# Performance work log

Hardware: AMD Instinct MI355X
Metric: run time of the kernel (lower is better)

The kernel has to match this reference:

```python
import jax, jax.numpy as jnp
import numpy as np

BN_EPS = 1e-5

def conv1x1(x, w, b):
    # x: [B,C,H,W], w: [O,C], b: [O]
    return jnp.einsum('bchw,oc->bohw', x, w) + b[None, :, None, None]

def bn_inf(x, gamma, beta, mean, var):
    inv = gamma / jnp.sqrt(var + BN_EPS)
    return (x - mean[None, :, None, None]) * inv[None, :, None, None] + beta[None, :, None, None]

def setup_inputs() -> dict:
    key = jax.random.key(0)
    ks = jax.random.split(key, 24)
    B, Fg, Fl, Fi = 8, 256, 256, 64
    H = W = 64
    c8 = Fi // 8
    d = {}
    d['g'] = jax.random.normal(ks[0], (B, Fg, H, W), jnp.float32)
    d['x'] = jax.random.normal(ks[1], (B, Fl, H, W), jnp.float32)
    # W_g: conv1x1 + BN
    d['Wg_w'] = jax.random.normal(ks[2], (Fi, Fg), jnp.float32) * (1.0 / np.sqrt(Fg))
    d['Wg_b'] = jax.random.normal(ks[3], (Fi,), jnp.float32) * 0.02
    d['bng_gamma'] = jax.random.uniform(ks[4], (Fi,), jnp.float32, 0.5, 1.5)
    d['bng_beta'] = jax.random.normal(ks[5], (Fi,), jnp.float32) * 0.1
    d['bng_mean'] = jax.random.normal(ks[6], (Fi,), jnp.float32) * 0.1
    d['bng_var'] = jax.random.uniform(ks[7], (Fi,), jnp.float32, 0.5, 1.5)
    # W_x: conv1x1 + BN
    d['Wx_w'] = jax.random.normal(ks[8], (Fi, Fl), jnp.float32) * (1.0 / np.sqrt(Fl))
    d['Wx_b'] = jax.random.normal(ks[9], (Fi,), jnp.float32) * 0.02
    d['bnx_gamma'] = jax.random.uniform(ks[10], (Fi,), jnp.float32, 0.5, 1.5)
    d['bnx_beta'] = jax.random.normal(ks[11], (Fi,), jnp.float32) * 0.1
    d['bnx_mean'] = jax.random.normal(ks[12], (Fi,), jnp.float32) * 0.1
    d['bnx_var'] = jax.random.uniform(ks[13], (Fi,), jnp.float32, 0.5, 1.5)
    # psi: conv1x1 (Fi->1) + BN(1) + sigmoid
    d['psi_w'] = jax.random.normal(ks[14], (1, Fi), jnp.float32) * (1.0 / np.sqrt(Fi))
    d['psi_b'] = jax.random.normal(ks[15], (1,), jnp.float32) * 0.02
    d['bnp_gamma'] = jax.random.uniform(ks[16], (1,), jnp.float32, 0.5, 1.5)
    d['bnp_beta'] = jax.random.normal(ks[17], (1,), jnp.float32) * 0.1
    d['bnp_mean'] = jax.random.normal(ks[18], (1,), jnp.float32) * 0.1
    d['bnp_var'] = jax.random.uniform(ks[19], (1,), jnp.float32, 0.5, 1.5)
    # PAM convs
    d['pb_w'] = jax.random.normal(ks[20], (c8, Fi), jnp.float32) * (1.0 / np.sqrt(Fi))
    d['pb_b'] = jnp.zeros((c8,), jnp.float32)
    d['pc_w'] = jax.random.normal(ks[21], (c8, Fi), jnp.float32) * (1.0 / np.sqrt(Fi))
    d['pc_b'] = jnp.zeros((c8,), jnp.float32)
    d['pd_w'] = jax.random.normal(ks[22], (Fi, Fi), jnp.float32) * (1.0 / np.sqrt(Fi))
    d['pd_b'] = jnp.zeros((Fi,), jnp.float32)
    # scalar gates (torch inits to 0; use small nonzero to exercise the path)
    d['alpha'] = jax.random.normal(ks[23], (1,), jnp.float32) * 0.05
    d['cam_beta'] = jax.random.normal(jax.random.fold_in(key, 99), (1,), jnp.float32) * 0.05
    return d

def _cam(psi, cam_beta):
    B, C, H, W = psi.shape
    feat = psi.reshape(B, C, H * W)                       # [B,C,HW]
    att = jnp.einsum('bcn,bdn->bcd', feat, feat)          # [B,C,C]
    att_new = jnp.max(att, axis=-1, keepdims=True) - att  # max-subtract trick
    att = jax.nn.softmax(att_new, axis=-1)
    out = jnp.einsum('bcd,bdn->bcn', att, feat).reshape(B, C, H, W)
    return cam_beta[0] * out + psi

def _pam(psi, pb_w, pb_b, pc_w, pc_b, pd_w, pd_b, alpha):
    B, C, H, W = psi.shape
    HW = H * W
    fb = conv1x1(psi, pb_w, pb_b).reshape(B, -1, HW)      # [B,C/8,HW]
    fc = conv1x1(psi, pc_w, pc_b).reshape(B, -1, HW)      # [B,C/8,HW]
    energy = jnp.einsum('bki,bkj->bij', fb, fc)           # [B,HW,HW]
    att = jax.nn.softmax(energy, axis=-1)
    fd = conv1x1(psi, pd_w, pd_b).reshape(B, C, HW)       # [B,C,HW]
    out = jnp.einsum('bcj,bij->bci', fd, att).reshape(B, C, H, W)
    return alpha[0] * out + psi

def reference(g, x, Wg_w, Wg_b, bng_gamma, bng_beta, bng_mean, bng_var,
              Wx_w, Wx_b, bnx_gamma, bnx_beta, bnx_mean, bnx_var,
              psi_w, psi_b, bnp_gamma, bnp_beta, bnp_mean, bnp_var,
              pb_w, pb_b, pc_w, pc_b, pd_w, pd_b, alpha, cam_beta):
    g1 = bn_inf(conv1x1(g, Wg_w, Wg_b), bng_gamma, bng_beta, bng_mean, bng_var)
    x1 = bn_inf(conv1x1(x, Wx_w, Wx_b), bnx_gamma, bnx_beta, bnx_mean, bnx_var)
    psi = jax.nn.relu(g1 + x1)                            # [B,F_int,H,W]
    cam = _cam(psi, cam_beta)
    pam = _pam(psi, pb_w, pb_b, pc_w, pc_b, pd_w, pd_b, alpha)
    gate = bn_inf(conv1x1(cam * pam, psi_w, psi_b), bnp_gamma, bnp_beta, bnp_mean, bnp_var)
    da = jax.nn.sigmoid(gate)                             # [B,1,H,W]
    return x * da
```

## Files before the change

kernel.cpp:

```cpp
#include <hip/hip_runtime.h>
#include <hip/hip_bf16.h>
#include <math.h>

#define BB 8
#define CIN 256
#define FI 64
#define HW 4096
#define C8 8
#define EPS 1e-5f
#define LOG2E 1.4426950408889634f

typedef __attribute__((ext_vector_type(8))) short bf16x8;
typedef __attribute__((ext_vector_type(4))) float f32x4;
typedef __attribute__((ext_vector_type(4))) unsigned u32x4;
typedef unsigned short u16;

static __device__ __forceinline__ u16 f2b(float x) {
    unsigned u = __builtin_bit_cast(unsigned, x);
    return (u16)((u + 0x8000u) >> 16);
}
static __device__ __forceinline__ unsigned pk2(float a, float b) {
    unsigned ua = __builtin_bit_cast(unsigned, a);
    unsigned ub = __builtin_bit_cast(unsigned, b);
    return ((ua + 0x8000u) >> 16) | ((ub + 0x8000u) & 0xffff0000u);
}
static __device__ __forceinline__ unsigned cvtpk(float a, float b) {
    unsigned r;
    asm("v_cvt_pk_bf16_f32 %0, %1, %2" : "=v"(r) : "v"(a), "v"(b));
    return r;
}
static __device__ __forceinline__ float b2f(u16 v) {
    return __builtin_bit_cast(float, ((unsigned)v) << 16);
}

__global__ __launch_bounds__(256) void k_prep(
    const float* __restrict__ Wg, const float* __restrict__ Wgb,
    const float* __restrict__ gg, const float* __restrict__ gbeta,
    const float* __restrict__ gm, const float* __restrict__ gv,
    const float* __restrict__ Wx, const float* __restrict__ Wxb,
    const float* __restrict__ xg, const float* __restrict__ xbeta,
    const float* __restrict__ xm, const float* __restrict__ xv,
    const float* __restrict__ pbw, const float* __restrict__ pbb,
    const float* __restrict__ pcw, const float* __restrict__ pcb,
    const float* __restrict__ pdw, const float* __restrict__ pdb,
    u16* __restrict__ Wp, float* __restrict__ Cp,
    u16* __restrict__ Wcat, float* __restrict__ bcat)
{
    const int gid = blockIdx.x * 256 + threadIdx.x;
    for (int idx = gid; idx < FI * 512; idx += 4096) {
        int o = idx >> 9, k = idx & 511;
        float s, w;
        if (k < 256) { s = gg[o] * rsqrtf(gv[o] + EPS); w = Wg[o * 256 + k]; }
        else         { s = xg[o] * rsqrtf(xv[o] + EPS); w = Wx[o * 256 + k - 256]; }
        Wp[idx] = f2b(w * s);
    }
    for (int idx = gid; idx < 80 * 64; idx += 4096) {
        int row = idx >> 6, col = idx & 63;
        float w;
        if (row < 8)       w = pbw[row * 64 + col] * LOG2E;
        else if (row < 16) w = pcw[(row - 8) * 64 + col];
        else               w = pdw[(row - 16) * 64 + col];
        Wcat[idx] = f2b(w);
    }
    if (blockIdx.x == 0) {
        int tid = threadIdx.x;
        if (tid < FI) {
            float ig = gg[tid] * rsqrtf(gv[tid] + EPS);
            float ix = xg[tid] * rsqrtf(xv[tid] + EPS);
            Cp[tid] = (Wgb[tid] - gm[tid]) * ig + gbeta[tid]
                    + (Wxb[tid] - xm[tid]) * ix + xbeta[tid];
        }
        if (tid >= 64 && tid < 144) {
            int r = tid - 64;
            float bv = (r < 8) ? pbb[r] * LOG2E : (r < 16 ? pcb[r - 8] : pdb[r - 16]);
            bcat[r] = bv;
        }
    }
}

__global__ __launch_bounds__(256) void k_psi(
    const float* __restrict__ g, const float* __restrict__ x,
    const u16* __restrict__ Wp, const float* __restrict__ Cp,
    const u16* __restrict__ Wcat, const float* __restrict__ bcat,
    u16* __restrict__ psiB, u16* __restrict__ psiLo,
    u16* __restrict__ fbcT, u16* __restrict__ fdB,
    u16* __restrict__ psiT, u16* __restrict__ psiTLo)
{
    const int tid  = threadIdx.x;
    const int lane = tid & 63;
    const int w    = tid >> 6;
    const int n    = lane & 15;
    const int quad = lane >> 4;
    const int b    = blockIdx.y;
    const int p0   = blockIdx.x * 64;

    __shared__ u16 InT[64][72];
    __shared__ u16 TpH[64][72];
    __shared__ u16 TpL[64][72];
    __shared__ u16 Tbc[64][16];

    f32x4 acc[4];
#pragma unroll
    for (int mt = 0; mt < 4; ++mt) acc[mt] = (f32x4){0.f, 0.f, 0.f, 0.f};

    const size_t pxoff = (size_t)p0 + w * 16 + n;
#pragma unroll
    for (int kc = 0; kc < 8; ++kc) {
        const float* src = (kc < 4) ? g : x;
        const int ch0 = (kc & 3) * 64;
        const float* base = src + ((size_t)b * CIN + ch0 + quad * 8) * HW + pxoff;
#pragma unroll
        for (int ks = 0; ks < 2; ++ks) {
            const float* bp = base + (size_t)(ks * 32) * HW;
            float f0 = bp[0 * HW], f1 = bp[1 * HW], f2 = bp[2 * HW], f3 = bp[3 * HW];
            float f4 = bp[4 * HW], f5 = bp[5 * HW], f6 = bp[6 * HW], f7 = bp[7 * HW];
            u32x4 t = {pk2(f0, f1), pk2(f2, f3), pk2(f4, f5), pk2(f6, f7)};
            bf16x8 bfrag = __builtin_bit_cast(bf16x8, t);
            const int kglob = kc * 64 + ks * 32;
#pragma unroll
            for (int mt = 0; mt < 4; ++mt) {
                bf16x8 af = *(const bf16x8*)&Wp[(mt * 16 + n) * 512 + kglob + quad * 8];
                acc[mt] = __builtin_amdgcn_mfma_f32_16x16x32_bf16(
                              af, bfrag, acc[mt], 0, 0, 0);
            }
        }
    }

    float pv[4][4];
    unsigned hbv[4][4], lov[4][4];
#pragma unroll
    for (int mt = 0; mt < 4; ++mt)
#pragma unroll
        for (int r = 0; r < 4; ++r) {
            int c = mt * 16 + quad * 4 + r;
            float v = acc[mt][r] + Cp[c];
            v = v > 0.f ? v : 0.f;
            pv[mt][r] = v;
            u16 hb = f2b(v);
            u16 lo = f2b(v - b2f(hb));
            hbv[mt][r] = hb;
            lov[mt][r] = lo;
            size_t idx = ((size_t)b * FI + c) * HW + p0 + w * 16 + n;
            psiB[idx]  = hb;
            psiLo[idx] = lo;
        }
#pragma unroll
    for (int mt = 0; mt < 4; ++mt) {
        *(unsigned*)&InT[w * 16 + n][mt * 16 + quad * 4]     = cvtpk(pv[mt][0], pv[mt][1]);
        *(unsigned*)&InT[w * 16 + n][mt * 16 + quad * 4 + 2] = cvtpk(pv[mt][2], pv[mt][3]);
        *(unsigned*)&TpH[w * 16 + n][mt * 16 + quad * 4]     = hbv[mt][0] | (hbv[mt][1] << 16);
        *(unsigned*)&TpH[w * 16 + n][mt * 16 + quad * 4 + 2] = hbv[mt][2] | (hbv[mt][3] << 16);
        *(unsigned*)&TpL[w * 16 + n][mt * 16 + quad * 4]     = lov[mt][0] | (lov[mt][1] << 16);
        *(unsigned*)&TpL[w * 16 + n][mt * 16 + quad * 4 + 2] = lov[mt][2] | (lov[mt][3] << 16);
    }
    __syncthreads();

    if (psiT != nullptr) {
#pragma unroll
        for (int rep = 0; rep < 2; ++rep) {
            int t = rep * 256 + tid;
            int row = t >> 3, seg = t & 7;
            size_t o = ((size_t)b * HW + p0 + row) * 64 + seg * 8;
            *(bf16x8*)&psiT[o]   = *(const bf16x8*)&TpH[row][seg * 8];
            *(bf16x8*)&psiTLo[o] = *(const bf16x8*)&TpL[row][seg * 8];
        }
    }

    f32x4 facc[5];
#pragma unroll
    for (int nt = 0; nt < 5; ++nt) facc[nt] = (f32x4){0.f, 0.f, 0.f, 0.f};
#pragma unroll
    for (int ks = 0; ks < 2; ++ks) {
        bf16x8 af = *(const bf16x8*)&InT[w * 16 + n][ks * 32 + quad * 8];
#pragma unroll
        for (int nt = 0; nt < 5; ++nt) {
            bf16x8 bf = *(const bf16x8*)&Wcat[(nt * 16 + n) * FI + ks * 32 + quad * 8];
            facc[nt] = __builtin_amdgcn_mfma_f32_16x16x32_bf16(af, bf, facc[nt], 0, 0, 0);
        }
    }
    __syncthreads();

    {
        float bias = bcat[n];
#pragma unroll
        for (int r = 0; r < 4; ++r)
            Tbc[w * 16 + quad * 4 + r][n] = f2b(facc[0][r] + bias);
    }
#pragma unroll
    for (int nt = 1; nt < 5; ++nt) {
        int ch = (nt - 1) * 16 + n;
        float bias = bcat[nt * 16 + n];
        *(unsigned*)&InT[ch][w * 16 + quad * 4]     = cvtpk(facc[nt][0] + bias, facc[nt][1] + bias);
        *(unsigned*)&InT[ch][w * 16 + quad * 4 + 2] = cvtpk(facc[nt][2] + bias, facc[nt][3] + bias);
    }
    __syncthreads();
    {
        int row = tid >> 2, part = tid & 3;
        uint2 v = *(const uint2*)&Tbc[row][part * 4];
        *(uint2*)&fbcT[((size_t)b * HW + p0 + row) * 16 + part * 4] = v;
    }
#pragma unroll
    for (int rep = 0; rep < 2; ++rep) {
        int t = rep * 256 + tid;
        int ch = t >> 3, seg = t & 7;
        bf16x8 v = *(const bf16x8*)&InT[ch][seg * 8];
        *(bf16x8*)&fdB[((size_t)b * FI + ch) * HW + p0 + seg * 8] = v;
    }
}

static __device__ __forceinline__ void gram_body(
    int tid, int s, int b, int zz,
    const u16* __restrict__ psiB, const u16* __restrict__ psiLo,
    float* __restrict__ Gp)
{
    const int lane = tid & 63;
    const int w    = tid >> 6;
    const int n    = lane & 15;
    const int quad = lane >> 4;

    f32x4 acc[2];
#pragma unroll
    for (int nt = 0; nt < 2; ++nt) acc[nt] = (f32x4){0.f, 0.f, 0.f, 0.f};

    for (int ks = 0; ks < 4; ++ks) {
        const int k0 = s * 128 + ks * 32;
        const size_t ra = ((size_t)b * FI + w * 16 + n) * HW + k0 + quad * 8;
        bf16x8 ah = *(const bf16x8*)&psiB[ra];
        bf16x8 al = *(const bf16x8*)&psiLo[ra];
#pragma unroll
        for (int nt = 0; nt < 2; ++nt) {
            const size_t rb = ((size_t)b * FI + zz * 32 + nt * 16 + n) * HW + k0 + quad * 8;
            bf16x8 bh = *(const bf16x8*)&psiB[rb];
            bf16x8 bl = *(const bf16x8*)&psiLo[rb];
            acc[nt] = __builtin_amdgcn_mfma_f32_16x16x32_bf16(ah, bh, acc[nt], 0, 0, 0);
            acc[nt] = __builtin_amdgcn_mfma_f32_16x16x32_bf16(ah, bl, acc[nt], 0, 0, 0);
            acc[nt] = __builtin_amdgcn_mfma_f32_16x16x32_bf16(al, bh, acc[nt], 0, 0, 0);
        }
    }
#pragma unroll
    for (int nt = 0; nt < 2; ++nt)
#pragma unroll
        for (int r = 0; r < 4; ++r) {
            int i = w * 16 + quad * 4 + r;
            Gp[(((size_t)s * 8 + b) * 64 + i) * 64 + zz * 32 + nt * 16 + n] = acc[nt][r];
        }
}

struct PamShared {
    u16 Ks[2][68][8];
    u16 Vs[2][64][64];
    u16 Ps[4][16][64];
};

template<int P>
static __device__ __forceinline__ void pam_body(
    PamShared& sh, int tid, int b, int i0, int p,
    const u16* __restrict__ fbcT, const u16* __restrict__ fdB,
    u16* __restrict__ Opart, float* __restrict__ ml)
{
    const int lane = tid & 63;
    const int w    = tid >> 6;
    const int n    = lane & 15;
    const int quad = lane >> 4;
    constexpr int JPER = 64 / P;
    const int jstart = p * JPER, jend = jstart + JPER;

    if (tid < 16) {
        ((unsigned*)&sh.Ks[0][64][0])[tid] = 0u;
        ((unsigned*)&sh.Ks[1][64][0])[tid] = 0u;
    }

    bf16x8 qfrag = {};
    if (quad == 0)
        qfrag = *(const bf16x8*)&fbcT[((size_t)b * HW + i0 + w * 16 + n) * 16];

    const int kkey = tid >> 1, khalf = tid & 1;
    const int vch  = tid >> 3, vseg  = tid & 7;
    const int vslot = (vseg ^ (vch & 7)) << 3;
    const int pswz  = n & 7;

    const u16* kp = fbcT + ((size_t)b * HW + jstart * 64) * 16 + 8;
    const u16* vp = fdB + (size_t)b * FI * HW + jstart * 64;

    uint2 kr0 = make_uint2(0u, 0u), kr1 = make_uint2(0u, 0u);
    bf16x8 v0a, v0b, v1a, v1b;
    if (tid < 128) {
        kr0 = *(const uint2*)(kp + (size_t)kkey * 16 + khalf * 4);
        kr1 = *(const uint2*)(kp + 1024 + (size_t)kkey * 16 + khalf * 4);
    }
    v0a = *(const bf16x8*)(vp + (size_t)vch * HW + vseg * 8);
    v0b = *(const bf16x8*)(vp + (size_t)(32 + vch) * HW + vseg * 8);
    v1a = *(const bf16x8*)(vp + 64 + (size_t)vch * HW + vseg * 8);
    v1b = *(const bf16x8*)(vp + 64 + (size_t)(32 + vch) * HW + vseg * 8);

    f32x4 oacc[4];
#pragma unroll
    for (int mt = 0; mt < 4; ++mt) oacc[mt] = (f32x4){0.f, 0.f, 0.f, 0.f};
    float m = -1e30f, l = 0.f;

#define PAM_STEP(BUF)                                                           \
    {                                                                           \
        f32x4 s[4];                                                             \
        __builtin_amdgcn_s_setprio(1);                                          \
        _Pragma("unroll")                                                       \
        for (int mt = 0; mt < 4; ++mt) {                                        \
            bf16x8 af = *(const bf16x8*)&sh.Ks[BUF][mt * 16 + n + quad][0];     \
            s[mt] = __builtin_amdgcn_mfma_f32_16x16x32_bf16(                    \
                        af, qfrag, (f32x4){0.f, 0.f, 0.f, 0.f}, 0, 0, 0);       \
        }                                                                       \
        __builtin_amdgcn_s_setprio(0);                                          \
        float cm = fmaxf(fmaxf(s[0][0], s[0][1]), s[0][2]);                     \
        cm = fmaxf(fmaxf(cm, s[0][3]), s[1][0]);                                \
        cm = fmaxf(fmaxf(cm, s[1][1]), s[1][2]);                                \
        cm = fmaxf(fmaxf(cm, s[1][3]), s[2][0]);                                \
        cm = fmaxf(fmaxf(cm, s[2][1]), s[2][2]);                                \
        cm = fmaxf(fmaxf(cm, s[2][3]), s[3][0]);                                \
        cm = fmaxf(fmaxf(cm, s[3][1]), s[3][2]);                                \
        cm = fmaxf(cm, s[3][3]);                                                \
        cm = fmaxf(cm, __shfl_xor(cm, 16));                                     \
        cm = fmaxf(cm, __shfl_xor(cm, 32));                                     \
        if (__any(cm > m + 8.f)) {                                              \
            float mnew  = fmaxf(m, cm);                                         \
            float scale = __builtin_amdgcn_exp2f(m - mnew);                     \
            l *= scale;                                                         \
            _Pragma("unroll")                                                   \
            for (int mt = 0; mt < 4; ++mt) {                                    \
                oacc[mt][0] *= scale; oacc[mt][1] *= scale;                     \
                oacc[mt][2] *= scale; oacc[mt][3] *= scale;                     \
            }                                                                   \
            m = mnew;                                                           \
        }                                                                       \
        float psum = 0.f;                                                       \
        unsigned pw[4][2];                                                      \
        _Pragma("unroll")                                                       \
        for (int mt = 0; mt < 4; ++mt) {                                        \
            float e0 = __builtin_amdgcn_exp2f(s[mt][0] - m);                    \
            float e1 = __builtin_amdgcn_exp2f(s[mt][1] - m);                    \
            float e2 = __builtin_amdgcn_exp2f(s[mt][2] - m);                    \
            float e3 = __builtin_amdgcn_exp2f(s[mt][3] - m);                    \
            psum += (e0 + e1) + (e2 + e3);                                      \
            pw[mt][0] = cvtpk(e0, e1);                                          \
            pw[mt][1] = cvtpk(e2, e3);                                          \
        }                                                                       \
        l += psum;                                                              \
        _Pragma("unroll")                                                       \
        for (int mt = 0; mt < 4; ++mt) {                                        \
            int so = (((mt * 2 + (quad >> 1)) ^ pswz) << 3) + ((quad & 1) << 2);\
            *(uint2*)&sh.Ps[w][n][so] = make_uint2(pw[mt][0], pw[mt][1]);       \
        }                                                                       \
        __builtin_amdgcn_s_setprio(1);                                          \
        _Pragma("unroll")                                                       \
        for (int k0 = 0; k0 < 2; ++k0) {                                        \
            bf16x8 pf = *(const bf16x8*)&sh.Ps[w][n][((k0 * 4 + quad) ^ pswz) << 3];\
            _Pragma("unroll")                                                   \
            for (int mt = 0; mt < 4; ++mt) {                                    \
                bf16x8 vf = *(const bf16x8*)                                    \
                    &sh.Vs[BUF][mt * 16 + n][((k0 * 4 + quad) ^ pswz) << 3];    \
                oacc[mt] = __builtin_amdgcn_mfma_f32_16x16x32_bf16(             \
                               vf, pf, oacc[mt], 0, 0, 0);                      \
            }                                                                   \
        }                                                                       \
        __builtin_amdgcn_s_setprio(0);                                          \
    }

    for (int jc = jstart; jc < jend; jc += 2) {
        if (tid < 128) *(uint2*)&sh.Ks[0][kkey][khalf * 4] = kr0;
        *(bf16x8*)&sh.Vs[0][vch][vslot]      = v0a;
        *(bf16x8*)&sh.Vs[0][32 + vch][vslot] = v0b;
        if (jc + 2 < jend) {
            if (tid < 128)
                kr0 = *(const uint2*)(kp + 2048 + (size_t)kkey * 16 + khalf * 4);
            v0a = *(const bf16x8*)(vp + 128 + (size_t)vch * HW + vseg * 8);
            v0b = *(const bf16x8*)(vp + 128 + (size_t)(32 + vch) * HW + vseg * 8);
        }
        __syncthreads();
        PAM_STEP(0)

        if (tid < 128) *(uint2*)&sh.Ks[1][kkey][khalf * 4] = kr1;
        *(bf16x8*)&sh.Vs[1][vch][vslot]      = v1a;
        *(bf16x8*)&sh.Vs[1][32 + vch][vslot] = v1b;
        if (jc + 3 < jend) {
            if (tid < 128)
                kr1 = *(const uint2*)(kp + 3072 + (size_t)kkey * 16 + khalf * 4);
            v1a = *(const bf16x8*)(vp + 192 + (size_t)vch * HW + vseg * 8);
            v1b = *(const bf16x8*)(vp + 192 + (size_t)(32 + vch) * HW + vseg * 8);
        }
        kp += 2048;
        vp += 128;
        __syncthreads();
        PAM_STEP(1)
    }
#undef PAM_STEP

    l += __shfl_xor(l, 16);
    l += __shfl_xor(l, 32);
    const float rl = 1.f / l;
#pragma unroll
    for (int mt = 0; mt < 4; ++mt)
#pragma unroll
        for (int r = 0; r < 4; ++r) {
            int c = mt * 16 + quad * 4 + r;
            Opart[(((size_t)p * 8 + b) * FI + c) * HW + i0 + w * 16 + n] =
                f2b(oacc[mt][r] * rl);
        }
    if (quad == 0)
        ((float2*)ml)[((size_t)p * 8 + b) * HW + i0 + w * 16 + n] = make_float2(m, l);
}

__global__ __launch_bounds__(256) void k_pamgram(
    const u16* __restrict__ fbcT, const u16* __restrict__ fdB,
    const u16* __restrict__ psiB, const u16* __restrict__ psiLo,
    u16* __restrict__ Opart, float* __restrict__ ml, float* __restrict__ Gp)
{
    __shared__ PamShared sh;
    const int bid = blockIdx.x;
    const int tid = threadIdx.x;
    if (bid < 512) {
        gram_body(tid, bid & 31, (bid >> 5) & 7, bid >> 8, psiB, psiLo, Gp);
    } else {
        const int pid = bid - 512;
        pam_body<2>(sh, tid, pid & 7, ((pid >> 3) & 63) * 64, pid >> 9,
                    fbcT, fdB, Opart, ml);
    }
}

__global__ __launch_bounds__(256) void k_gram(
    const u16* __restrict__ psiB, const u16* __restrict__ psiLo,
    float* __restrict__ Gp)
{
    gram_body(threadIdx.x, blockIdx.x, blockIdx.y, blockIdx.z, psiB, psiLo, Gp);
}
__global__ __launch_bounds__(256) void k_pam(
    const u16* __restrict__ fbcT, const u16* __restrict__ fdB,
    u16* __restrict__ Opart, float* __restrict__ ml)
{
    __shared__ PamShared sh;
    pam_body<2>(sh, threadIdx.x, blockIdx.x, blockIdx.y * 64, blockIdx.z,
                fbcT, fdB, Opart, ml);
}

__global__ __launch_bounds__(256) void k_camsm(
    const float* __restrict__ Gp, float* __restrict__ att)
{
    const int tid = threadIdx.x, tx = tid & 63, ty = tid >> 6;
    const int b = blockIdx.x, i = blockIdx.y;
    __shared__ float part[4][64];

    float gs = 0.f;
#pragma unroll
    for (int j = 0; j < 8; ++j) {
        int s = ty * 8 + j;
        gs += Gp[(((size_t)s * 8 + b) * 64 + i) * 64 + tx];
    }
    part[ty][tx] = gs;
    __syncthreads();
    if (tid < 64) {
        float gsum = part[0][tx] + part[1][tx] + part[2][tx] + part[3][tx];
        float M = gsum;
#pragma unroll
        for (int msk = 1; msk < 64; msk <<= 1) M = fmaxf(M, __shfl_xor(M, msk));
        float a = M - gsum;
        float m2 = a;
#pragma unroll
        for (int msk = 1; msk < 64; msk <<= 1) m2 = fmaxf(m2, __shfl_xor(m2, msk));
        float p = __expf(a - m2);
        float ssum = p;
#pragma unroll
        for (int msk = 1; msk < 64; msk <<= 1) ssum += __shfl_xor(ssum, msk);
        att[((size_t)b * 64 + i) * 64 + tx] = p / ssum;
    }
}

__global__ __launch_bounds__(256) void k_final_v(
    const u16* __restrict__ psiT, const u16* __restrict__ psiTLo,
    const float* __restrict__ att,
    const u16* __restrict__ Opart, const float* __restrict__ ml,
    const float* __restrict__ x,
    const float* __restrict__ psiw, const float* __restrict__ psib,
    const float* __restrict__ pg, const float* __restrict__ pbeta,
    const float* __restrict__ pm, const float* __restrict__ pv,
    const float* __restrict__ alpha, const float* __restrict__ camb,
    float* __restrict__ out)
{
    const int tid  = threadIdx.x;
    const int lane = tid & 63;
    const int w    = tid >> 6;
    const int n    = lane & 15;
    const int quad = lane >> 4;
    const int b = blockIdx.y, p0 = blockIdx.x * 32;

    __shared__ u16 Abf[64][64];
    __shared__ u16 tpB[32][64];
    __shared__ u16 tpLo[32][64];
    __shared__ u16 OpS[2][64][40];
    __shared__ float Wc[2][32];
    __shared__ float Pw[64];
    __shared__ alignas(16) float daL[32];
    __shared__ float Zp[4][32];

    {
        int c = tid >> 2, seg = tid & 3;
        const float* ap = &att[((size_t)b * 64 + c) * 64 + seg * 16];
        float4 v0 = *(const float4*)(ap);
        float4 v1 = *(const float4*)(ap + 4);
        float4 v2 = *(const float4*)(ap + 8);
        float4 v3 = *(const float4*)(ap + 12);
        float vv[16] = {v0.x, v0.y, v0.z, v0.w, v1.x, v1.y, v1.z, v1.w,
                        v2.x, v2.y, v2.z, v2.w, v3.x, v3.y, v3.z, v3.w};
#pragma unroll
        for (int j = 0; j < 8; ++j) {
            int d0 = seg * 16 + j * 2;
            int phys = (((d0 >> 3) ^ (c & 7)) << 3) | (d0 & 7);
            *(unsigned*)&Abf[c][phys] = cvtpk(vv[2 * j], vv[2 * j + 1]);
        }
    }
    {
        int row = tid >> 3, seg = tid & 7;
        size_t o = ((size_t)b * HW + p0 + row) * 64 + seg * 8;
        int phys = ((seg ^ (row & 7)) << 3);
        *(bf16x8*)&tpB[row][phys]  = *(const bf16x8*)&psiT[o];
        *(bf16x8*)&tpLo[row][phys] = *(const bf16x8*)&psiTLo[o];
    }
#pragma unroll
    for (int rep = 0; rep < 2; ++rep) {
        int cid = rep * 256 + tid;
        int pp = cid >> 8, c = (cid >> 2) & 63, sg = cid & 3;
        *(bf16x8*)&OpS[pp][c][sg * 8] =
            *(const bf16x8*)&Opart[(((size_t)pp * 8 + b) * FI + c) * HW + p0 + sg * 8];
    }
    if (tid < 64) Pw[tid] = psiw[tid];
    if (tid < 32) {
        float2 ml0 = ((const float2*)ml)[((size_t)0 * 8 + b) * HW + p0 + tid];
        float2 ml1 = ((const float2*)ml)[((size_t)1 * 8 + b) * HW + p0 + tid];
        float M  = fmaxf(ml0.x, ml1.x);
        float w0 = ml0.y * __builtin_amdgcn_exp2f(ml0.x - M);
        float w1 = ml1.y * __builtin_amdgcn_exp2f(ml1.x - M);
        float winv = 1.f / (w0 + w1);
        Wc[0][tid] = w0 * winv; Wc[1][tid] = w1 * winv;
    }
    __syncthreads();

    f32x4 acc[2];
#pragma unroll
    for (int nt = 0; nt < 2; ++nt) acc[nt] = (f32x4){0.f, 0.f, 0.f, 0.f};
#pragma unroll
    for (int ks = 0; ks < 2; ++ks) {
        int arow = w * 16 + n;
        bf16x8 af = *(const bf16x8*)&Abf[arow][((ks * 4 + quad) ^ (arow & 7)) << 3];
#pragma unroll
        for (int nt = 0; nt < 2; ++nt) {
            int brow = nt * 16 + n;
            int boff = ((ks * 4 + quad) ^ (brow & 7)) << 3;
            bf16x8 bh = *(const bf16x8*)&tpB[brow][boff];
            bf16x8 bl = *(const bf16x8*)&tpLo[brow][boff];
            acc[nt] = __builtin_amdgcn_mfma_f32_16x16x32_bf16(af, bh, acc[nt], 0, 0, 0);
            acc[nt] = __builtin_amdgcn_mfma_f32_16x16x32_bf16(af, bl, acc[nt], 0, 0, 0);
        }
    }

    const float al = alpha[0], cb = camb[0];
    float z[2] = {0.f, 0.f};
#pragma unroll
    for (int nt = 0; nt < 2; ++nt) {
        int px = nt * 16 + n;
        float w0 = Wc[0][px], w1 = Wc[1][px];
#pragma unroll
        for (int r = 0; r < 4; ++r) {
            int c = w * 16 + quad * 4 + r;
            int phys = (((c >> 3) ^ (px & 7)) << 3) | (c & 7);
            float ps  = b2f(tpB[px][phys]) + b2f(tpLo[px][phys]);
            float cam = cb * acc[nt][r] + ps;
            float oa = w0 * b2f(OpS[0][c][px]) + w1 * b2f(OpS[1][c][px]);
            float pam = al * oa + ps;
            z[nt] += Pw[c] * (cam * pam);
        }
    }
#pragma unroll
    for (int nt = 0; nt < 2; ++nt) {
        z[nt] += __shfl_xor(z[nt], 16);
        z[nt] += __shfl_xor(z[nt], 32);
    }
    if (quad == 0) {
#pragma unroll
        for (int nt = 0; nt < 2; ++nt) Zp[w][nt * 16 + n] = z[nt];
    }
    __syncthreads();
    if (tid < 32) {
        float zt = Zp[0][tid] + Zp[1][tid] + Zp[2][tid] + Zp[3][tid] + psib[0];
        float inv = pg[0] * rsqrtf(pv[0] + EPS);
        float gate = (zt - pm[0]) * inv + pbeta[0];
        daL[tid] = 1.f / (1.f + __expf(-gate));
    }
    __syncthreads();

    {
        const int pxg = tid & 7, chb = tid >> 3;
        float4 daf = *(const float4*)&daL[pxg * 4];
#pragma unroll
        for (int r = 0; r < 8; ++r) {
            int cl = chb + 32 * r;
            size_t idx = ((size_t)b * CIN + cl) * HW + p0 + pxg * 4;
            float4 xv = *(const float4*)&x[idx];
            *(float4*)&out[idx] = make_float4(xv.x * daf.x, xv.y * daf.y,
                                              xv.z * daf.z, xv.w * daf.w);
        }
    }
}

__global__ __launch_bounds__(256) void k_final_s(
    const u16* __restrict__ psiB, const u16* __restrict__ psiLo,
    const float* __restrict__ att,
    const u16* __restrict__ Opart, const float* __restrict__ ml,
    const float* __restrict__ x,
    const float* __restrict__ psiw, const float* __restrict__ psib,
    const float* __restrict__ pg, const float* __restrict__ pbeta,
    const float* __restrict__ pm, const float* __restrict__ pv,
    const float* __restrict__ alpha, const float* __restrict__ camb,
    float* __restrict__ out)
{
    const int tid  = threadIdx.x;
    const int lane = tid & 63;
    const int w    = tid >> 6;
    const int n    = lane & 15;
    const int quad = lane >> 4;
    const int b = blockIdx.y, p0 = blockIdx.x * 64;

    __shared__ u16 Abf[64][64];
    __shared__ u16 tpB[64][64];
    __shared__ u16 tpLo[64][64];
    __shared__ float Wc0[64], Wc1[64], Pw[64];
    __shared__ alignas(16) float daL[64];
    __shared__ float Zp[4][64];

    {
        int c = tid >> 2, seg = tid & 3;
        const float* ap = &att[((size_t)b * 64 + c) * 64 + seg * 16];
        float4 v0 = *(const float4*)(ap);
        float4 v1 = *(const float4*)(ap + 4);
        float4 v2 = *(const float4*)(ap + 8);
        float4 v3 = *(const float4*)(ap + 12);
        float vv[16] = {v0.x, v0.y, v0.z, v0.w, v1.x, v1.y, v1.z, v1.w,
                        v2.x, v2.y, v2.z, v2.w, v3.x, v3.y, v3.z, v3.w};
#pragma unroll
        for (int j = 0; j < 8; ++j) {
            int d0 = seg * 16 + j * 2;
            int phys = (((d0 >> 3) ^ (c & 7)) << 3) | (d0 & 7);
            *(unsigned*)&Abf[c][phys] = cvtpk(vv[2 * j], vv[2 * j + 1]);
        }
    }
    {
        int px = tid & 63, grp = tid >> 6;
#pragma unroll
        for (int cc = 0; cc < 16; cc += 2) {
            int c = grp * 16 + cc;
            size_t i0 = ((size_t)b * FI + c) * HW + p0 + px;
            unsigned hb = ((unsigned)psiB[i0]) | (((unsigned)psiB[i0 + HW]) << 16);
            unsigned lb = ((unsigned)psiLo[i0]) | (((unsigned)psiLo[i0 + HW]) << 16);
            int phys = (((c >> 3) ^ (px & 7)) << 3) | (c & 7);
            *(unsigned*)&tpB[px][phys]  = hb;
            *(unsigned*)&tpLo[px][phys] = lb;
        }
    }
    if (tid < 64) {
        Pw[tid] = psiw[tid];
        float2 ml0 = ((const float2*)ml)[((size_t)0 * 8 + b) * HW + p0 + tid];
        float2 ml1 = ((const float2*)ml)[((size_t)1 * 8 + b) * HW + p0 + tid];
        float M  = fmaxf(ml0.x, ml1.x);
        float w0 = ml0.y * __builtin_amdgcn_exp2f(ml0.x - M);
        float w1 = ml1.y * __builtin_amdgcn_exp2f(ml1.x - M);
        float winv = 1.f / (w0 + w1);
        Wc0[tid] = w0 * winv; Wc1[tid] = w1 * winv;
    }
    __syncthreads();

    f32x4 acc[4];
#pragma unroll
    for (int nt = 0; nt < 4; ++nt) acc[nt] = (f32x4){0.f, 0.f, 0.f, 0.f};
#pragma unroll
    for (int ks = 0; ks < 2; ++ks) {
        int arow = w * 16 + n;
        bf16x8 af = *(const bf16x8*)&Abf[arow][((ks * 4 + quad) ^ (arow & 7)) << 3];
#pragma unroll
        for (int nt = 0; nt < 4; ++nt) {
            int brow = nt * 16 + n;
            int boff = ((ks * 4 + quad) ^ (brow & 7)) << 3;
            bf16x8 bh = *(const bf16x8*)&tpB[brow][boff];
            bf16x8 bl = *(const bf16x8*)&tpLo[brow][boff];
            acc[nt] = __builtin_amdgcn_mfma_f32_16x16x32_bf16(af, bh, acc[nt], 0, 0, 0);
            acc[nt] = __builtin_amdgcn_mfma_f32_16x16x32_bf16(af, bl, acc[nt], 0, 0, 0);
        }
    }

    const float al = alpha[0], cb = camb[0];
    float z[4] = {0.f, 0.f, 0.f, 0.f};
#pragma unroll
    for (int nt = 0; nt < 4; ++nt) {
        int px = nt * 16 + n;
        float w0 = Wc0[px], w1 = Wc1[px];
#pragma unroll
        for (int r = 0; r < 4; ++r) {
            int c = w * 16 + quad * 4 + r;
            int phys = (((c >> 3) ^ (px & 7)) << 3) | (c & 7);
            float ps  = b2f(tpB[px][phys]) + b2f(tpLo[px][phys]);
            float cam = cb * acc[nt][r] + ps;
            float oa = w0 * b2f(Opart[(((size_t)0 * 8 + b) * FI + c) * HW + p0 + px])
                     + w1 * b2f(Opart[(((size_t)1 * 8 + b) * FI + c) * HW + p0 + px]);
            float pam = al * oa + ps;
            z[nt] += Pw[c] * (cam * pam);
        }
    }
#pragma unroll
    for (int nt = 0; nt < 4; ++nt) {
        z[nt] += __shfl_xor(z[nt], 16);
        z[nt] += __shfl_xor(z[nt], 32);
    }
    if (quad == 0) {
#pragma unroll
        for (int nt = 0; nt < 4; ++nt) Zp[w][nt * 16 + n] = z[nt];
    }
    __syncthreads();
    if (tid < 64) {
        float zt = Zp[0][tid] + Zp[1][tid] + Zp[2][tid] + Zp[3][tid] + psib[0];
        float inv = pg[0] * rsqrtf(pv[0] + EPS);
        float gate = (zt - pm[0]) * inv + pbeta[0];
        daL[tid] = 1.f / (1.f + __expf(-gate));
    }
    __syncthreads();

    {
        const int pxg = tid & 15, chb = tid >> 4;
        float4 daf = *(const float4*)&daL[pxg * 4];
#pragma unroll
        for (int r = 0; r < 16; ++r) {
            int cl = chb + 16 * r;
            size_t idx = ((size_t)b * CIN + cl) * HW + p0 + pxg * 4;
            float4 xv = *(const float4*)&x[idx];
            *(float4*)&out[idx] = make_float4(xv.x * daf.x, xv.y * daf.y,
                                              xv.z * daf.z, xv.w * daf.w);
        }
    }
}

extern "C" void kernel_launch(void* const* d_in, const int* in_sizes, int n_in,
                              void* d_out, int out_size, void* d_ws, size_t ws_size,
                              hipStream_t stream)
{
    const float* g     = (const float*)d_in[0];
    const float* x     = (const float*)d_in[1];
    const float* Wg_w  = (const float*)d_in[2];
    const float* Wg_b  = (const float*)d_in[3];
    const float* bng_g = (const float*)d_in[4];
    const float* bng_b = (const float*)d_in[5];
    const float* bng_m = (const float*)d_in[6];
    const float* bng_v = (const float*)d_in[7];
    const float* Wx_w  = (const float*)d_in[8];
    const float* Wx_b  = (const float*)d_in[9];
    const float* bnx_g = (const float*)d_in[10];
    const float* bnx_b = (const float*)d_in[11];
    const float* bnx_m = (const float*)d_in[12];
    const float* bnx_v = (const float*)d_in[13];
    const float* psi_w = (const float*)d_in[14];
    const float* psi_b = (const float*)d_in[15];
    const float* bnp_g = (const float*)d_in[16];
    const float* bnp_b = (const float*)d_in[17];
    const float* bnp_m = (const float*)d_in[18];
    const float* bnp_v = (const float*)d_in[19];
    const float* pb_w  = (const float*)d_in[20];
    const float* pb_b  = (const float*)d_in[21];
    const float* pc_w  = (const float*)d_in[22];
    const float* pc_b  = (const float*)d_in[23];
    const float* pd_w  = (const float*)d_in[24];
    const float* pd_b  = (const float*)d_in[25];
    const float* alpha = (const float*)d_in[26];
    const float* camb  = (const float*)d_in[27];
    float* out = (float*)d_out;

    float* ws   = (float*)d_ws;
    u16*  psiB   = (u16*)(ws);
    u16*  psiLo  = (u16*)(ws + 1048576);
    u16*  fbcT   = (u16*)(ws + 2097152);
    u16*  fdB    = (u16*)(ws + 2359296);
    float* att   = ws + 3407872;
    u16*  Wp     = (u16*)(ws + 3440640);
    float* Cp    = ws + 3457024;
    u16*  Wcat   = (u16*)(ws + 3457088);
    float* bcat  = ws + 3459648;
    float* mlws  = ws + 3459744;
    float* Gp    = ws + 3590816;
    u16*  psiT   = (u16*)(ws + 6736544);
    u16*  psiTL  = (u16*)(ws + 7785120);

    const bool wsB = ws_size >= (size_t)6736544 * 4;
    const bool wsA = ws_size >= (size_t)8833696 * 4;
    u16* Opart = wsB ? (u16*)(ws + 4639392)
                     : (u16*)(ws + 3590816);

    k_prep<<<dim3(16), 256, 0, stream>>>(Wg_w, Wg_b, bng_g, bng_b, bng_m, bng_v,
                                         Wx_w, Wx_b, bnx_g, bnx_b, bnx_m, bnx_v,
                                         pb_w, pb_b, pc_w, pc_b, pd_w, pd_b,
                                         Wp, Cp, Wcat, bcat);
    k_psi<<<dim3(64, 8), 256, 0, stream>>>(g, x, Wp, Cp, Wcat, bcat,
                                           psiB, psiLo, fbcT, fdB,
                                           wsA ? psiT : nullptr,
                                           wsA ? psiTL : nullptr);
    if (wsB) {
        k_pamgram<<<dim3(1536), 256, 0, stream>>>(fbcT, fdB, psiB, psiLo,
                                                  Opart, mlws, Gp);
        k_camsm<<<dim3(8, 64), 256, 0, stream>>>(Gp, att);
    } else {
        k_gram<<<dim3(32, 8, 2), 256, 0, stream>>>(psiB, psiLo, Gp);
        k_camsm<<<dim3(8, 64), 256, 0, stream>>>(Gp, att);
        k_pam<<<dim3(8, 64, 2), 256, 0, stream>>>(fbcT, fdB, Opart, mlws);
    }
    if (wsA) {
        k_final_v<<<dim3(128, 8), 256, 0, stream>>>(psiT, psiTL, att, Opart, mlws, x,
                                                    psi_w, psi_b, bnp_g, bnp_b,
                                                    bnp_m, bnp_v, alpha, camb, out);
    } else {
        k_final_s<<<dim3(64, 8), 256, 0, stream>>>(psiB, psiLo, att, Opart, mlws, x,
                                                   psi_w, psi_b, bnp_g, bnp_b,
                                                   bnp_m, bnp_v, alpha, camb, out);
    }
}
```

Before: 245.0 us.

## Process two query tiles per PAM block to reuse K/V shared tiles

Each PAM attention block now handles 128 query rows (two 64-row tiles with separate online-softmax state), so every K/V tile loaded into shared memory feeds twice as many MFMAs, and grids are halved accordingly. The aim is to cut global/LDS traffic for K and V per unit of work and amortize loop overhead. It costs more registers (two accumulator sets) and doubled P shared buffer, and leaves fewer blocks for parallelism. Separately, the psi conv bf16 packing switches from manual rounding to the hardware v_cvt_pk_bf16_f32 instruction.

Result: slower. 252.0 us (+2.8%).

```diff
diff --git a/kernel.cpp b/kernel.cpp
--- a/kernel.cpp
+++ b/kernel.cpp
@@ -18,11 +18,6 @@
 static __device__ __forceinline__ u16 f2b(float x) {
     unsigned u = __builtin_bit_cast(unsigned, x);
     return (u16)((u + 0x8000u) >> 16);
-}
-static __device__ __forceinline__ unsigned pk2(float a, float b) {
-    unsigned ua = __builtin_bit_cast(unsigned, a);
-    unsigned ub = __builtin_bit_cast(unsigned, b);
-    return ((ua + 0x8000u) >> 16) | ((ub + 0x8000u) & 0xffff0000u);
 }
 static __device__ __forceinline__ unsigned cvtpk(float a, float b) {
     unsigned r;
@@ -114,7 +109,7 @@
             const float* bp = base + (size_t)(ks * 32) * HW;
             float f0 = bp[0 * HW], f1 = bp[1 * HW], f2 = bp[2 * HW], f3 = bp[3 * HW];
             float f4 = bp[4 * HW], f5 = bp[5 * HW], f6 = bp[6 * HW], f7 = bp[7 * HW];
-            u32x4 t = {pk2(f0, f1), pk2(f2, f3), pk2(f4, f5), pk2(f6, f7)};
+            u32x4 t = {cvtpk(f0, f1), cvtpk(f2, f3), cvtpk(f4, f5), cvtpk(f6, f7)};
             bf16x8 bfrag = __builtin_bit_cast(bf16x8, t);
             const int kglob = kc * 64 + ks * 32;
 #pragma unroll
@@ -249,7 +244,7 @@
 struct PamShared {
     u16 Ks[2][68][8];
     u16 Vs[2][64][64];
-    u16 Ps[4][16][64];
+    u16 Ps[2][4][16][64];
 };
 
 template<int P>
@@ -270,9 +265,11 @@
         ((unsigned*)&sh.Ks[1][64][0])[tid] = 0u;
     }
 
-    bf16x8 qfrag = {};
-    if (quad == 0)
-        qfrag = *(const bf16x8*)&fbcT[((size_t)b * HW + i0 + w * 16 + n) * 16];
+    bf16x8 qfragA = {}, qfragB = {};
+    if (quad == 0) {
+        qfragA = *(const bf16x8*)&fbcT[((size_t)b * HW + i0 + w * 16 + n) * 16];
+        qfragB = *(const bf16x8*)&fbcT[((size_t)b * HW + i0 + 64 + w * 16 + n) * 16];
+    }
 
     const int kkey = tid >> 1, khalf = tid & 1;
     const int vch  = tid >> 3, vseg  = tid & 7;
@@ -293,12 +290,15 @@
     v1a = *(const bf16x8*)(vp + 64 + (size_t)vch * HW + vseg * 8);
     v1b = *(const bf16x8*)(vp + 64 + (size_t)(32 + vch) * HW + vseg * 8);
 
-    f32x4 oacc[4];
-#pragma unroll
-    for (int mt = 0; mt < 4; ++mt) oacc[mt] = (f32x4){0.f, 0.f, 0.f, 0.f};
-    float m = -1e30f, l = 0.f;
-
-#define PAM_STEP(BUF)                                                           \
+    f32x4 oaccA[4], oaccB[4];
+#pragma unroll
+    for (int mt = 0; mt < 4; ++mt) {
+        oaccA[mt] = (f32x4){0.f, 0.f, 0.f, 0.f};
+        oaccB[mt] = (f32x4){0.f, 0.f, 0.f, 0.f};
+    }
+    float mA = -1e30f, lA = 0.f, mB = -1e30f, lB = 0.f;
+
+#define QKSM(BUF, QF, PSIDX, M, L, OACC)                                        \
     {                                                                           \
         f32x4 s[4];                                                             \
         __builtin_amdgcn_s_setprio(1);                                          \
@@ -306,7 +306,7 @@
         for (int mt = 0; mt < 4; ++mt) {                                        \
             bf16x8 af = *(const bf16x8*)&sh.Ks[BUF][mt * 16 + n + quad][0];     \
             s[mt] = __builtin_amdgcn_mfma_f32_16x16x32_bf16(                    \
-                        af, qfrag, (f32x4){0.f, 0.f, 0.f, 0.f}, 0, 0, 0);       \
+                        af, QF, (f32x4){0.f, 0.f, 0.f, 0.f}, 0, 0, 0);          \
         }                                                                       \
         __builtin_amdgcn_s_setprio(0);                                          \
         float cm = fmaxf(fmaxf(s[0][0], s[0][1]), s[0][2]);                     \
@@ -319,45 +319,54 @@
         cm = fmaxf(cm, s[3][3]);                                                \
         cm = fmaxf(cm, __shfl_xor(cm, 16));                                     \
         cm = fmaxf(cm, __shfl_xor(cm, 32));                                     \
-        if (__any(cm > m + 8.f)) {                                              \
-            float mnew  = fmaxf(m, cm);                                         \
-            float scale = __builtin_amdgcn_exp2f(m - mnew);                     \
-            l *= scale;                                                         \
+        if (__any(cm > M + 8.f)) {                                              \
+            float mnew  = fmaxf(M, cm);                                         \
+            float scale = __builtin_amdgcn_exp2f(M - mnew);                     \
+            L *= scale;                                                         \
             _Pragma("unroll")                                                   \
             for (int mt = 0; mt < 4; ++mt) {                                    \
-                oacc[mt][0] *= scale; oacc[mt][1] *= scale;                     \
-                oacc[mt][2] *= scale; oacc[mt][3] *= scale;                     \
+                OACC[mt][0] *= scale; OACC[mt][1] *= scale;                     \
+                OACC[mt][2] *= scale; OACC[mt][3] *= scale;                     \
             }                                                                   \
-            m = mnew;                                                           \
+            M = mnew;                                                           \
         }                                                                       \
         float psum = 0.f;                                                       \
         unsigned pw[4][2];                                                      \
         _Pragma("unroll")                                                       \
         for (int mt = 0; mt < 4; ++mt) {                                        \
-            float e0 = __builtin_amdgcn_exp2f(s[mt][0] - m);                    \
-            float e1 = __builtin_amdgcn_exp2f(s[mt][1] - m);                    \
-            float e2 = __builtin_amdgcn_exp2f(s[mt][2] - m);                    \
-            float e3 = __builtin_amdgcn_exp2f(s[mt][3] - m);                    \
+            float e0 = __builtin_amdgcn_exp2f(s[mt][0] - M);                    \
+            float e1 = __builtin_amdgcn_exp2f(s[mt][1] - M);                    \
+            float e2 = __builtin_amdgcn_exp2f(s[mt][2] - M);                    \
+            float e3 = __builtin_amdgcn_exp2f(s[mt][3] - M);                    \
             psum += (e0 + e1) + (e2 + e3);                                      \
             pw[mt][0] = cvtpk(e0, e1);                                          \
             pw[mt][1] = cvtpk(e2, e3);                                          \
         }                                                                       \
-        l += psum;                                                              \
+        L += psum;                                                              \
         _Pragma("unroll")                                                       \
         for (int mt = 0; mt < 4; ++mt) {                                        \
             int so = (((mt * 2 + (quad >> 1)) ^ pswz) << 3) + ((quad & 1) << 2);\
-            *(uint2*)&sh.Ps[w][n][so] = make_uint2(pw[mt][0], pw[mt][1]);       \
+            *(uint2*)&sh.Ps[PSIDX][w][n][so] = make_uint2(pw[mt][0], pw[mt][1]);\
         }                                                                       \
+    }
+
+#define PAM_STEP(BUF)                                                           \
+    {                                                                           \
+        QKSM(BUF, qfragA, 0, mA, lA, oaccA)                                     \
+        QKSM(BUF, qfragB, 1, mB, lB, oaccB)                                     \
         __builtin_amdgcn_s_setprio(1);                                          \
         _Pragma("unroll")                                                       \
         for (int k0 = 0; k0 < 2; ++k0) {                                        \
-            bf16x8 pf = *(const bf16x8*)&sh.Ps[w][n][((k0 * 4 + quad) ^ pswz) << 3];\
+            int po = ((k0 * 4 + quad) ^ pswz) << 3;                             \
+            bf16x8 pfA = *(const bf16x8*)&sh.Ps[0][w][n][po];                   \
+            bf16x8 pfB = *(const bf16x8*)&sh.Ps[1][w][n][po];                   \
             _Pragma("unroll")                                                   \
             for (int mt = 0; mt < 4; ++mt) {                                    \
-                bf16x8 vf = *(const bf16x8*)                                    \
-                    &sh.Vs[BUF][mt * 16 + n][((k0 * 4 + quad) ^ pswz) << 3];    \
-                oacc[mt] = __builtin_amdgcn_mfma_f32_16x16x32_bf16(             \
-                               vf, pf, oacc[mt], 0, 0, 0);                      \
+                bf16x8 vf = *(const bf16x8*)&sh.Vs[BUF][mt * 16 + n][po];       \
+                oaccA[mt] = __builtin_amdgcn_mfma_f32_16x16x32_bf16(            \
+                                vf, pfA, oaccA[mt], 0, 0, 0);                   \
+                oaccB[mt] = __builtin_amdgcn_mfma_f32_16x16x32_bf16(            \
+                                vf, pfB, oaccB[mt], 0, 0, 0);                   \
             }                                                                   \
         }                                                                       \
         __builtin_amdgcn_s_setprio(0);                                          \
@@ -391,20 +400,26 @@
         PAM_STEP(1)
     }
 #undef PAM_STEP
-
-    l += __shfl_xor(l, 16);
-    l += __shfl_xor(l, 32);
-    const float rl = 1.f / l;
+#undef QKSM
+
+    lA += __shfl_xor(lA, 16);
+    lA += __shfl_xor(lA, 32);
+    lB += __shfl_xor(lB, 16);
+    lB += __shfl_xor(lB, 32);
+    const float rlA = 1.f / lA, rlB = 1.f / lB;
 #pragma unroll
     for (int mt = 0; mt < 4; ++mt)
 #pragma unroll
         for (int r = 0; r < 4; ++r) {
             int c = mt * 16 + quad * 4 + r;
-            Opart[(((size_t)p * 8 + b) * FI + c) * HW + i0 + w * 16 + n] =
-                f2b(oacc[mt][r] * rl);
-        }
-    if (quad == 0)
-        ((float2*)ml)[((size_t)p * 8 + b) * HW + i0 + w * 16 + n] = make_float2(m, l);
+            size_t base = (((size_t)p * 8 + b) * FI + c) * HW + w * 16 + n;
+            Opart[base + i0]      = f2b(oaccA[mt][r] * rlA);
+            Opart[base + i0 + 64] = f2b(oaccB[mt][r] * rlB);
+        }
+    if (quad == 0) {
+        ((float2*)ml)[((size_t)p * 8 + b) * HW + i0 + w * 16 + n]      = make_float2(mA, lA);
+        ((float2*)ml)[((size_t)p * 8 + b) * HW + i0 + 64 + w * 16 + n] = make_float2(mB, lB);
+    }
 }
 
 __global__ __launch_bounds__(256) void k_pamgram(
@@ -419,7 +434,7 @@
         gram_body(tid, bid & 31, (bid >> 5) & 7, bid >> 8, psiB, psiLo, Gp);
     } else {
         const int pid = bid - 512;
-        pam_body<2>(sh, tid, pid & 7, ((pid >> 3) & 63) * 64, pid >> 9,
+        pam_body<2>(sh, tid, pid & 7, ((pid >> 3) & 31) * 128, pid >> 8,
                     fbcT, fdB, Opart, ml);
     }
 }
@@ -435,7 +450,7 @@
     u16* __restrict__ Opart, float* __restrict__ ml)
 {
     __shared__ PamShared sh;
-    pam_body<2>(sh, threadIdx.x, blockIdx.x, blockIdx.y * 64, blockIdx.z,
+    pam_body<2>(sh, threadIdx.x, blockIdx.x, blockIdx.y * 128, blockIdx.z,
                 fbcT, fdB, Opart, ml);
 }
 
@@ -804,13 +819,13 @@
                                            wsA ? psiT : nullptr,
                                            wsA ? psiTL : nullptr);
     if (wsB) {
-        k_pamgram<<<dim3(1536), 256, 0, stream>>>(fbcT, fdB, psiB, psiLo,
+        k_pamgram<<<dim3(1024), 256, 0, stream>>>(fbcT, fdB, psiB, psiLo,
                                                   Opart, mlws, Gp);
         k_camsm<<<dim3(8, 64), 256, 0, stream>>>(Gp, att);
     } else {
         k_gram<<<dim3(32, 8, 2), 256, 0, stream>>>(psiB, psiLo, Gp);
         k_camsm<<<dim3(8, 64), 256, 0, stream>>>(Gp, att);
-        k_pam<<<dim3(8, 64, 2), 256, 0, stream>>>(fbcT, fdB, Opart, mlws);
+        k_pam<<<dim3(8, 32, 2), 256, 0, stream>>>(fbcT, fdB, Opart, mlws);
     }
     if (wsA) {
         k_final_v<<<dim3(128, 8), 256, 0, stream>>>(psiT, psiTL, att, Opart, mlws, x,
```
